# Optimization experiments

Hardware: AMD Instinct MI355X
Metric: run time of the kernel (lower is better)

The kernel has to match this reference:

```python
import jax, jax.numpy as jnp
import numpy as np

# PyTorch bicubic (a=-0.75), half-pixel coords, scale factor 2 -> fixed fractional
# offset t=0.5 for every output pixel, giving constant taps at src offsets [-1,0,1,2].
CUBIC_W = np.array([-0.09375, 0.59375, 0.59375, -0.09375], dtype=np.float32)


def _down_last(x):
    """Bicubic 2x downsample along the last axis (PyTorch semantics, border clamp)."""
    n = x.shape[-1]
    no = n // 2
    idx = jnp.clip(2 * jnp.arange(no)[:, None] + jnp.arange(-1, 3)[None, :], 0, n - 1)  # (no,4)
    g = x[..., idx]  # (..., no, 4)
    return jnp.einsum('...ok,k->...o', g, jnp.asarray(CUBIC_W, dtype=x.dtype))


def _downsample_bicubic(x):
    # separable: width then height (order irrelevant)
    x = _down_last(x)
    x = jnp.swapaxes(x, -1, -2)
    x = _down_last(x)
    return jnp.swapaxes(x, -1, -2)


def _fftpack_hilbert(x):
    """scipy.fftpack.hilbert: y_j = 1j*sign(j)*x_j in Fourier space, Nyquist zeroed."""
    n = x.shape[0]
    X = np.fft.fft(x)
    sgn = np.zeros(n)
    sgn[1:n // 2] = 1.0
    sgn[n // 2 + 1:] = -1.0
    return np.real(np.fft.ifft(1j * sgn * X))


def _db8_filters():
    gl = np.array([-0.00011747678400228192, 0.0006754494059985568, -0.0003917403729959771,
                   -0.00487035299301066, 0.008746094047015655, 0.013981027917015516,
                   -0.04408825393106472, -0.01736930100202211, 0.128747426620186,
                   0.00047248457399797254, -0.2840155429624281, -0.015829105256023893,
                   0.5853546836548691, 0.6756307362980128, 0.3128715909144659,
                   0.05441584224308161])
    gh = np.array([-0.05441584224308161, 0.3128715909144659, -0.6756307362980128,
                   0.5853546836548691, 0.015829105256023893, -0.2840155429624281,
                   -0.00047248457399797254, 0.128747426620186, 0.01736930100202211,
                   -0.04408825393106472, -0.013981027917015516, 0.008746094047015655,
                   0.00487035299301066, -0.0003917403729959771, -0.0006754494059985568,
                   -0.00011747678400228192])
    fl = _fftpack_hilbert(gl)
    fh = _fftpack_hilbert(gh)
    return gl, gh, fl, fh


def setup_inputs() -> dict:
    key = jax.random.key(0)
    image = jax.random.normal(key, (4, 16, 512, 512), dtype=jnp.float32)
    gl, gh, fl, fh = _db8_filters()
    return {
        'image': image,
        'gl': jnp.asarray(gl, dtype=jnp.float32),
        'gh': jnp.asarray(gh, dtype=jnp.float32),
        'fl': jnp.asarray(fl, dtype=jnp.float32),
        'fh': jnp.asarray(fh, dtype=jnp.float32),
    }


def reference(image, gl, gh, fl, fh):
    # The original _column_convolve/_row_convolve never shift X (out += X*h[idx]),
    # so after the reflect-pad gather and centered slice, colfilter/rowfilter
    # reduce exactly to X * sum(h). Each sub-band is therefore
    # downsample(image) * sum(col_filter) * sum(row_filter).
    sg, sh = jnp.sum(gl), jnp.sum(gh)
    sfl, sfh = jnp.sum(fl), jnp.sum(fh)
    D = _downsample_bicubic(image)  # (B, C, H/2, W/2)
    LL = jnp.concatenate([D * (sg * sg), D * (sfl * sg), D * (sg * sfl), D * (sfl * sfl)], axis=1)
    b1 = jnp.concatenate([D * (sg * sh), D * (sfl * sh), D * (sg * sfh), D * (sfl * sfh)], axis=1)
    b2 = jnp.concatenate([D * (sh * sg), D * (sfh * sg), D * (sh * sfl), D * (sfh * sfl)], axis=1)
    b3 = jnp.concatenate([D * (sh * sh), D * (sfh * sh), D * (sh * sfh), D * (sfh * sfh)], axis=1)
    H = jnp.stack([b1, b2, b3], axis=2)  # (B, 4C, 3, H/2, W/2)
    return (LL, H)
```

## Files before the change

### kernel.cpp

```cpp
#include <hip/hip_runtime.h>

typedef float f32x4 __attribute__((ext_vector_type(4)));

__global__ void qwt_sums_kernel(const float* __restrict__ gl, const float* __restrict__ gh,
                                const float* __restrict__ fl, const float* __restrict__ fh,
                                float* __restrict__ ws) {
    int t = threadIdx.x;
    if (t < 4) {
        const float* p = (t == 0) ? gl : (t == 1) ? gh : (t == 2) ? fl : fh;
        float s = 0.f;
        #pragma unroll
        for (int i = 0; i < 16; i++) s += p[i];
        ws[t] = s;
    }
}

__global__ __launch_bounds__(256) void qwt_main_kernel(const float* __restrict__ img,
                                                       const float* __restrict__ ws,
                                                       float* __restrict__ out) {
    const float w0 = -0.09375f, w1 = 0.59375f;

    int t    = blockIdx.x * 256 + threadIdx.x;
    int lane = t & 63;
    int row  = t >> 6;
    int y    = row & 255;
    int bc   = row >> 8;
    int x0   = lane << 2;

    float sg = ws[0], sh = ws[1], sfl = ws[2], sfh = ws[3];

    const float* src = img + (size_t)bc * (512 * 512);

    float acc0 = 0.f, acc1 = 0.f, acc2 = 0.f, acc3 = 0.f;
    #pragma unroll
    for (int j = 0; j < 4; j++) {
        int ry = 2 * y - 1 + j;
        ry = ry < 0 ? 0 : (ry > 511 ? 511 : ry);
        const f32x4* rp4 = (const f32x4*)(src + (size_t)ry * 512);
        f32x4 v0 = rp4[2 * lane];
        f32x4 v1 = rp4[2 * lane + 1];
        float left  = __shfl_up(v1.w, 1);
        float right = __shfl_down(v0.x, 1);
        if (lane == 0)  left  = v0.x;
        if (lane == 63) right = v1.w;

        float h0 = w0 * left + w1 * v0.x + w1 * v0.y + w0 * v0.z;
        float h1 = w0 * v0.y + w1 * v0.z + w1 * v0.w + w0 * v1.x;
        float h2 = w0 * v0.w + w1 * v1.x + w1 * v1.y + w0 * v1.z;
        float h3 = w0 * v1.y + w1 * v1.z + w1 * v1.w + w0 * right;

        float wj = (j == 0 || j == 3) ? w0 : w1;
        acc0 += wj * h0; acc1 += wj * h1; acc2 += wj * h2; acc3 += wj * h3;
    }

    int b   = bc >> 4;
    int cc_ = bc & 15;
    size_t rowoff = ((size_t)y << 8) + (size_t)x0;
    const size_t P  = 65536;
    const size_t HB = 16777216;

    float* llp = out + ((size_t)(b * 64 + cc_)) * P + rowoff;
    float* hp  = out + HB + ((size_t)(b * 64 + cc_)) * 3 * P + rowoff;

    #pragma unroll
    for (int q = 0; q < 4; q++) {
        float f1g = (q & 1) ? sfl : sg;
        float f1h = (q & 1) ? sfh : sh;
        float f2g = (q & 2) ? sfl : sg;
        float f2h = (q & 2) ? sfh : sh;

        {
            float s = f1g * f2g;
            f32x4 v = {acc0 * s, acc1 * s, acc2 * s, acc3 * s};
            __builtin_nontemporal_store(v, (f32x4*)llp);
        }
        {
            float s = f1g * f2h;
            f32x4 v = {acc0 * s, acc1 * s, acc2 * s, acc3 * s};
            __builtin_nontemporal_store(v, (f32x4*)hp);
        }
        {
            float s = f1h * f2g;
            f32x4 v = {acc0 * s, acc1 * s, acc2 * s, acc3 * s};
            __builtin_nontemporal_store(v, (f32x4*)(hp + P));
        }
        {
            float s = f1h * f2h;
            f32x4 v = {acc0 * s, acc1 * s, acc2 * s, acc3 * s};
            __builtin_nontemporal_store(v, (f32x4*)(hp + 2 * P));
        }

        llp += 16 * P;
        hp  += 48 * P;
    }
}

extern "C" void kernel_launch(void* const* d_in, const int* in_sizes, int n_in,
                              void* d_out, int out_size, void* d_ws, size_t ws_size,
                              hipStream_t stream) {
    const float* img = (const float*)d_in[0];
    const float* gl  = (const float*)d_in[1];
    const float* gh  = (const float*)d_in[2];
    const float* fl  = (const float*)d_in[3];
    const float* fh  = (const float*)d_in[4];
    float* out = (float*)d_out;
    float* ws  = (float*)d_ws;

    qwt_sums_kernel<<<1, 64, 0, stream>>>(gl, gh, fl, fh, ws);
    qwt_main_kernel<<<4096, 256, 0, stream>>>(img, ws, out);
}
```

Measured before the change: 318.3 us.

## Compute four output rows per wave to reuse horizontally filtered source rows

Each wavefront now produces four consecutive output rows, loading ten source rows once and reusing the horizontal-filter results across the overlapping vertical taps, rather than reading four rows per output row. This cuts redundant global reads by about 2.5x and the grid shrinks fourfold. Stores switch from nontemporal to regular stores, which may change how the large output stream behaves in the cache. It also adds register pressure from holding 40 intermediate values.

```diff
diff --git a/kernel.cpp b/kernel.cpp
--- a/kernel.cpp
+++ b/kernel.cpp
@@ -22,21 +22,22 @@
 
     int t    = blockIdx.x * 256 + threadIdx.x;
     int lane = t & 63;
-    int row  = t >> 6;
-    int y    = row & 255;
-    int bc   = row >> 8;
+    int wid  = t >> 6;
+    int ygrp = wid & 63;
+    int bc   = wid >> 6;
+    int y0   = ygrp << 2;
     int x0   = lane << 2;
 
     float sg = ws[0], sh = ws[1], sfl = ws[2], sfh = ws[3];
 
     const float* src = img + (size_t)bc * (512 * 512);
 
-    float acc0 = 0.f, acc1 = 0.f, acc2 = 0.f, acc3 = 0.f;
+    float h[10][4];
     #pragma unroll
-    for (int j = 0; j < 4; j++) {
-        int ry = 2 * y - 1 + j;
-        ry = ry < 0 ? 0 : (ry > 511 ? 511 : ry);
-        const f32x4* rp4 = (const f32x4*)(src + (size_t)ry * 512);
+    for (int k = 0; k < 10; k++) {
+        int sr = 2 * y0 - 1 + k;
+        sr = sr < 0 ? 0 : (sr > 511 ? 511 : sr);
+        const f32x4* rp4 = (const f32x4*)(src + (size_t)sr * 512);
         f32x4 v0 = rp4[2 * lane];
         f32x4 v1 = rp4[2 * lane + 1];
         float left  = __shfl_up(v1.w, 1);
@@ -44,18 +45,26 @@
         if (lane == 0)  left  = v0.x;
         if (lane == 63) right = v1.w;
 
-        float h0 = w0 * left + w1 * v0.x + w1 * v0.y + w0 * v0.z;
-        float h1 = w0 * v0.y + w1 * v0.z + w1 * v0.w + w0 * v1.x;
-        float h2 = w0 * v0.w + w1 * v1.x + w1 * v1.y + w0 * v1.z;
-        float h3 = w0 * v1.y + w1 * v1.z + w1 * v1.w + w0 * right;
+        h[k][0] = w0 * left + w1 * v0.x + w1 * v0.y + w0 * v0.z;
+        h[k][1] = w0 * v0.y + w1 * v0.z + w1 * v0.w + w0 * v1.x;
+        h[k][2] = w0 * v0.w + w1 * v1.x + w1 * v1.y + w0 * v1.z;
+        h[k][3] = w0 * v1.y + w1 * v1.z + w1 * v1.w + w0 * right;
+    }
 
-        float wj = (j == 0 || j == 3) ? w0 : w1;
-        acc0 += wj * h0; acc1 += wj * h1; acc2 += wj * h2; acc3 += wj * h3;
+    f32x4 acc[4];
+    #pragma unroll
+    for (int r = 0; r < 4; r++) {
+        #pragma unroll
+        for (int i = 0; i < 4; i++) {
+            float a = w0 * h[2 * r][i] + w1 * h[2 * r + 1][i]
+                    + w1 * h[2 * r + 2][i] + w0 * h[2 * r + 3][i];
+            acc[r][i] = a;
+        }
     }
 
     int b   = bc >> 4;
     int cc_ = bc & 15;
-    size_t rowoff = ((size_t)y << 8) + (size_t)x0;
+    size_t rowoff = ((size_t)y0 << 8) + (size_t)x0;
     const size_t P  = 65536;
     const size_t HB = 16777216;
 
@@ -69,25 +78,30 @@
         float f2g = (q & 2) ? sfl : sg;
         float f2h = (q & 2) ? sfh : sh;
 
-        {
-            float s = f1g * f2g;
-            f32x4 v = {acc0 * s, acc1 * s, acc2 * s, acc3 * s};
-            __builtin_nontemporal_store(v, (f32x4*)llp);
+        float sLL = f1g * f2g;
+        float s0  = f1g * f2h;
+        float s1  = f1h * f2g;
+        float s2  = f1h * f2h;
+
+        #pragma unroll
+        for (int r = 0; r < 4; r++) {
+            f32x4 v = {acc[r][0] * sLL, acc[r][1] * sLL, acc[r][2] * sLL, acc[r][3] * sLL};
+            *(f32x4*)(llp + r * 256) = v;
         }
-        {
-            float s = f1g * f2h;
-            f32x4 v = {acc0 * s, acc1 * s, acc2 * s, acc3 * s};
-            __builtin_nontemporal_store(v, (f32x4*)hp);
+        #pragma unroll
+        for (int r = 0; r < 4; r++) {
+            f32x4 v = {acc[r][0] * s0, acc[r][1] * s0, acc[r][2] * s0, acc[r][3] * s0};
+            *(f32x4*)(hp + r * 256) = v;
         }
-        {
-            float s = f1h * f2g;
-            f32x4 v = {acc0 * s, acc1 * s, acc2 * s, acc3 * s};
-            __builtin_nontemporal_store(v, (f32x4*)(hp + P));
+        #pragma unroll
+        for (int r = 0; r < 4; r++) {
+            f32x4 v = {acc[r][0] * s1, acc[r][1] * s1, acc[r][2] * s1, acc[r][3] * s1};
+            *(f32x4*)(hp + P + r * 256) = v;
         }
-        {
-            float s = f1h * f2h;
-            f32x4 v = {acc0 * s, acc1 * s, acc2 * s, acc3 * s};
-            __builtin_nontemporal_store(v, (f32x4*)(hp + 2 * P));
+        #pragma unroll
+        for (int r = 0; r < 4; r++) {
+            f32x4 v = {acc[r][0] * s2, acc[r][1] * s2, acc[r][2] * s2, acc[r][3] * s2};
+            *(f32x4*)(hp + 2 * P + r * 256) = v;
         }
 
         llp += 16 * P;
@@ -107,5 +121,5 @@
     float* ws  = (float*)d_ws;
 
     qwt_sums_kernel<<<1, 64, 0, stream>>>(gl, gh, fl, fh, ws);
-    qwt_main_kernel<<<4096, 256, 0, stream>>>(img, ws, out);
+    qwt_main_kernel<<<1024, 256, 0, stream>>>(img, ws, out);
 }
```

Result: slower. 327.0 us (+2.7%).
